# Optimization experiments

Hardware: AMD Instinct MI355X
Metric: run time of the kernel (lower is better)

Reference implementation:

```python
import jax, jax.numpy as jnp
import numpy as np

OUT_H = OUT_W = 7
SCALE = 0.25
SR = 2  # sampling_ratio


def setup_inputs() -> dict:
    key = jax.random.key(0)
    k1, k2, k3, k4, k5, k6 = jax.random.split(key, 6)
    B, C, H, W = 2, 256, 200, 304
    N = 1000
    inputs = jax.random.normal(k1, (B, C, H, W), dtype=jnp.float32)
    # rois: (batch_idx, cx, cy, w, h, angle_deg) in IMAGE coords (scale back by 1/SCALE)
    bidx = jax.random.randint(k2, (N,), 0, B).astype(jnp.float32)
    cx = jax.random.uniform(k3, (N,), minval=0.0, maxval=W / SCALE)
    cy = jax.random.uniform(k4, (N,), minval=0.0, maxval=H / SCALE)
    wh = jax.random.uniform(k5, (N, 2), minval=16.0, maxval=256.0)
    ang = jax.random.uniform(k6, (N,), minval=-90.0, maxval=90.0)
    rois = jnp.concatenate([bidx[:, None], cx[:, None], cy[:, None], wh, ang[:, None]], axis=1)
    return {"inputs": inputs, "rois": rois}


def _roi_align_rotated(feats, rois):
    B, C, H, W = feats.shape
    N = rois.shape[0]
    offset = 0.5  # aligned=True continuous-coordinate convention
    bidx = rois[:, 0].astype(jnp.int32)
    cw = rois[:, 1] * SCALE - offset
    ch = rois[:, 2] * SCALE - offset
    rw = rois[:, 3] * SCALE
    rh = rois[:, 4] * SCALE
    theta = rois[:, 5] * (jnp.pi / 180.0)
    cos_t, sin_t = jnp.cos(theta), jnp.sin(theta)

    bin_h = rh / OUT_H
    bin_w = rw / OUT_W
    # fused (bin, subsample) coordinate: t[j] = ph + (iy+0.5)/SR for j = ph*SR+iy
    t_y = (jnp.arange(OUT_H * SR, dtype=feats.dtype) + 0.5) / SR  # [GH]
    t_x = (jnp.arange(OUT_W * SR, dtype=feats.dtype) + 0.5) / SR  # [GW]
    yy = -rh[:, None] / 2.0 + t_y[None, :] * bin_h[:, None]  # [N,GH] roi-local
    xx = -rw[:, None] / 2.0 + t_x[None, :] * bin_w[:, None]  # [N,GW]

    # rotate into feature-map coords
    y = yy[:, :, None] * cos_t[:, None, None] - xx[:, None, :] * sin_t[:, None, None] + ch[:, None, None]
    x = yy[:, :, None] * sin_t[:, None, None] + xx[:, None, :] * cos_t[:, None, None] + cw[:, None, None]

    empty = (y < -1.0) | (y > H) | (x < -1.0) | (x > W)
    y = jnp.clip(y, 0.0, None)
    x = jnp.clip(x, 0.0, None)
    y_low = jnp.clip(jnp.floor(y).astype(jnp.int32), 0, H - 1)
    x_low = jnp.clip(jnp.floor(x).astype(jnp.int32), 0, W - 1)
    y_high = jnp.minimum(y_low + 1, H - 1)
    x_high = jnp.minimum(x_low + 1, W - 1)
    ly = jnp.clip(y - y_low.astype(y.dtype), 0.0, 1.0)
    lx = jnp.clip(x - x_low.astype(x.dtype), 0.0, 1.0)
    hy, hx = 1.0 - ly, 1.0 - lx

    b = bidx[:, None, None]  # [N,1,1] broadcasts with [N,GH,GW] index arrays
    v1 = feats[b, :, y_low, x_low]    # [N,GH,GW,C]
    v2 = feats[b, :, y_low, x_high]
    v3 = feats[b, :, y_high, x_low]
    v4 = feats[b, :, y_high, x_high]

    w1 = (hy * hx)[..., None]
    w2 = (hy * lx)[..., None]
    w3 = (ly * hx)[..., None]
    w4 = (ly * lx)[..., None]
    val = w1 * v1 + w2 * v2 + w3 * v3 + w4 * v4  # [N,GH,GW,C]
    val = jnp.where(empty[..., None], 0.0, val)

    # average the SRxSR samples within each output bin
    val = val.reshape(rois.shape[0], OUT_H, SR, OUT_W, SR, C).mean(axis=(2, 4))
    return jnp.transpose(val, (0, 3, 1, 2))  # [N,C,OUT_H,OUT_W]


def reference(inputs, rois):
    return _roi_align_rotated(inputs, rois)
```

## Files before the change

kernel.cpp:

```cpp
#include <hip/hip_runtime.h>
#include <math.h>

constexpr int Bn = 2, Cn = 256, Hn = 200, Wn = 304, Nroi = 1000;
constexpr int OH = 7, OW = 7, SRn = 2;
constexpr int NS = OH * SRn;
constexpr int NP = NS * NS;
constexpr int NBIN = OH * OW;
constexpr int HWn = Hn * Wn;
constexpr float SCALE = 0.25f;

__device__ __forceinline__ void compute_desc(const float* __restrict__ r, int p,
                                             int& idx, int& dx, int& dyW,
                                             float4& w) {
  float cw = r[1] * SCALE - 0.5f;
  float ch = r[2] * SCALE - 0.5f;
  float rw = r[3] * SCALE;
  float rh = r[4] * SCALE;
  float theta = r[5] * 0.017453292519943295f;
  float cs = cosf(theta), sn = sinf(theta);
  float bin_h = rh * (1.0f / OH);
  float bin_w = rw * (1.0f / OW);
  int ki = p / NS;
  int kj = p - ki * NS;
  float ty = ((float)ki + 0.5f) * (1.0f / SRn);
  float tx = ((float)kj + 0.5f) * (1.0f / SRn);
  float yy = -0.5f * rh + ty * bin_h;
  float xx = -0.5f * rw + tx * bin_w;
  float y = yy * cs - xx * sn + ch;
  float x = yy * sn + xx * cs + cw;
  bool empty = (y < -1.0f) || (y > (float)Hn) || (x < -1.0f) || (x > (float)Wn);
  y = fmaxf(y, 0.0f);
  x = fmaxf(x, 0.0f);
  int yl = min(max((int)floorf(y), 0), Hn - 1);
  int xl = min(max((int)floorf(x), 0), Wn - 1);
  int yh = min(yl + 1, Hn - 1);
  int xh = min(xl + 1, Wn - 1);
  float ly = fminf(fmaxf(y - (float)yl, 0.0f), 1.0f);
  float lx = fminf(fmaxf(x - (float)xl, 0.0f), 1.0f);
  float hy = 1.0f - ly, hx = 1.0f - lx;
  if (empty) {
    w.x = w.y = w.z = w.w = 0.0f;
  } else {
    w.x = hy * hx;
    w.y = hy * lx;
    w.z = ly * hx;
    w.w = ly * lx;
  }
  idx = yl * Wn + xl;
  dx = xh - xl;
  dyW = (yh - yl) * Wn;
}

__device__ __forceinline__ unsigned bf16rne(float f) {
  unsigned u = __float_as_uint(f);
  return (u + 0x7fffu + ((u >> 16) & 1u)) >> 16;
}
__device__ __forceinline__ unsigned bf16pack(float lo, float hi) {
  return bf16rne(lo) | (bf16rne(hi) << 16);
}

__global__ __launch_bounds__(512) void sort_rois(const float* __restrict__ rois,
                                                 int* __restrict__ perm) {
  __shared__ unsigned a[1024];
  int t = threadIdx.x;
  for (int i = t; i < 1024; i += 512) {
    unsigned packed;
    if (i < Nroi) {
      const float* r = rois + (size_t)i * 6;
      int b = (int)r[0];
      int tx = min(max((int)(r[1] * SCALE * (1.0f / 16.0f)), 0), 31);
      int ty = min(max((int)(r[2] * SCALE * (1.0f / 16.0f)), 0), 31);
      unsigned m = 0;
#pragma unroll
      for (int bit = 0; bit < 5; ++bit) {
        m |= (((tx >> bit) & 1u) << (2 * bit)) | (((ty >> bit) & 1u) << (2 * bit + 1));
      }
      unsigned key = ((unsigned)b << 10) | m;
      packed = (key << 10) | (unsigned)i;
    } else {
      packed = 0xFFFFFC00u | (unsigned)i;
    }
    a[i] = packed;
  }
  for (int k = 2; k <= 1024; k <<= 1) {
    for (int j = k >> 1; j > 0; j >>= 1) {
      __syncthreads();
      int i = ((t & ~(j - 1)) << 1) | (t & (j - 1));
      bool up = ((i & k) == 0);
      unsigned x = a[i], y = a[i + j];
      if ((x > y) == up) {
        a[i] = y;
        a[i + j] = x;
      }
    }
  }
  __syncthreads();
  for (int i = t; i < Nroi; i += 512) perm[i] = (int)(a[i] & 1023u);
}

constexpr int TPX = 64, TCH = 64, LP = TPX + 1;
__global__ __launch_bounds__(256) void transpose_bf16(const float* __restrict__ feats,
                                                      unsigned short* __restrict__ ft) {
  __shared__ float tile[TCH * LP];
  int p0 = blockIdx.x * TPX;
  int c0 = blockIdx.y * TCH;
  int b = blockIdx.z;
  int t = threadIdx.x;
  int px4 = t & 15, ch = t >> 4;
#pragma unroll
  for (int i = 0; i < 4; ++i) {
    int c = ch + 16 * i;
    const float4 v = *(const float4*)(feats + ((size_t)b * Cn + c0 + c) * HWn + p0 + px4 * 4);
    tile[c * LP + px4 * 4 + 0] = v.x;
    tile[c * LP + px4 * 4 + 1] = v.y;
    tile[c * LP + px4 * 4 + 2] = v.z;
    tile[c * LP + px4 * 4 + 3] = v.w;
  }
  __syncthreads();
  int o = t & 7;
  int px8 = t >> 3;
#pragma unroll
  for (int pass = 0; pass < 2; ++pass) {
    int p = px8 + 32 * pass;
    uint4 w4;
    w4.x = bf16pack(tile[(o * 8 + 0) * LP + p], tile[(o * 8 + 1) * LP + p]);
    w4.y = bf16pack(tile[(o * 8 + 2) * LP + p], tile[(o * 8 + 3) * LP + p]);
    w4.z = bf16pack(tile[(o * 8 + 4) * LP + p], tile[(o * 8 + 5) * LP + p]);
    w4.w = bf16pack(tile[(o * 8 + 6) * LP + p], tile[(o * 8 + 7) * LP + p]);
    *(uint4*)((char*)ft + (((size_t)b * HWn + p0 + p) * Cn + c0 + o * 8) * 2) = w4;
  }
}

constexpr int BPX = 32;
constexpr int SEG = 125;
__global__ __launch_bounds__(512, 2) void roi_gather9(const unsigned short* __restrict__ ft,
                                                      const float* __restrict__ rois,
                                                      const int* __restrict__ perm,
                                                      float* __restrict__ out) {
  __shared__ int4 s_m[NP];
  __shared__ float4 s_w[NP];
  __shared__ __align__(16) float s_out[Cn * NBIN];
  int x = blockIdx.x & 7;
  int jb = blockIdx.x >> 3;
  int t = threadIdx.x;
  int lane = t & 63;
  int wv = t >> 6;
  int k = lane & 31;
  int q = lane >> 5;

  for (int step = 0; step < 4; ++step) {
    int idxr = step * BPX + jb;
    if (idxr >= SEG) break;
    int n = perm[x * SEG + idxr];
    const float* r = rois + (size_t)n * 6;
    if (t < NP) {
      int idx, dx, dy;
      float4 w;
      compute_desc(r, t, idx, dx, dy, w);
      s_m[t] = make_int4(idx * (Cn * 2), dx * (Cn * 2), dy * (Cn * 2), 0);
      s_w[t] = w;
    }
    __syncthreads();
    int b = (int)r[0];
    const char* fb = (const char*)ft + (size_t)b * HWn * Cn * 2 + (size_t)k * 16;

    for (int bin = wv; bin < NBIN; bin += 8) {
      int bi = bin / OW;
      int bj = bin - bi * OW;
      int p00 = (bi * 2) * NS + bj * 2;
      float acc0 = 0.f, acc1 = 0.f, acc2 = 0.f, acc3 = 0.f;
      float acc4 = 0.f, acc5 = 0.f, acc6 = 0.f, acc7 = 0.f;
#pragma unroll
      for (int s = 0; s < 4; ++s) {
        int p = p00 + (s >> 1) * NS + (s & 1);
        int4 m = s_m[p];
        float4 w = s_w[p];
        const char* A = fb + m.x + q * m.y;
        uint4 vlo = *(const uint4*)(A);
        uint4 vhi = *(const uint4*)(A + m.z);
        float wlo = q ? w.y : w.x;
        float whi = q ? w.w : w.z;
#define ACC(vv, ww)                                                        \
        acc0 += (ww) * __uint_as_float((vv).x << 16);                      \
        acc1 += (ww) * __uint_as_float((vv).x & 0xffff0000u);              \
        acc2 += (ww) * __uint_as_float((vv).y << 16);                      \
        acc3 += (ww) * __uint_as_float((vv).y & 0xffff0000u);              \
        acc4 += (ww) * __uint_as_float((vv).z << 16);                      \
        acc5 += (ww) * __uint_as_float((vv).z & 0xffff0000u);              \
        acc6 += (ww) * __uint_as_float((vv).w << 16);                      \
        acc7 += (ww) * __uint_as_float((vv).w & 0xffff0000u);
        ACC(vlo, wlo)
        ACC(vhi, whi)
#undef ACC
      }
      acc0 += __shfl_xor(acc0, 32);
      acc1 += __shfl_xor(acc1, 32);
      acc2 += __shfl_xor(acc2, 32);
      acc3 += __shfl_xor(acc3, 32);
      acc4 += __shfl_xor(acc4, 32);
      acc5 += __shfl_xor(acc5, 32);
      acc6 += __shfl_xor(acc6, 32);
      acc7 += __shfl_xor(acc7, 32);
      if (q == 0) {
        s_out[(k * 8 + 0) * NBIN + bin] = acc0 * 0.25f;
        s_out[(k * 8 + 1) * NBIN + bin] = acc1 * 0.25f;
        s_out[(k * 8 + 2) * NBIN + bin] = acc2 * 0.25f;
        s_out[(k * 8 + 3) * NBIN + bin] = acc3 * 0.25f;
        s_out[(k * 8 + 4) * NBIN + bin] = acc4 * 0.25f;
        s_out[(k * 8 + 5) * NBIN + bin] = acc5 * 0.25f;
        s_out[(k * 8 + 6) * NBIN + bin] = acc6 * 0.25f;
        s_out[(k * 8 + 7) * NBIN + bin] = acc7 * 0.25f;
      }
    }
    __syncthreads();
    float* ob = out + (size_t)n * Cn * NBIN;
    for (int i = t; i < Cn * NBIN; i += 512) ob[i] = s_out[i];
    __syncthreads();
  }
}

__global__ __launch_bounds__(256) void roi_direct(const float* __restrict__ feats,
                                                  const float* __restrict__ rois,
                                                  float* __restrict__ out) {
  __shared__ int s_idx[NP];
  __shared__ int s_dx[NP];
  __shared__ int s_dy[NP];
  __shared__ float4 s_w[NP];
  int n = blockIdx.x;
  const float* r = rois + (size_t)n * 6;
  int t = threadIdx.x;
  if (t < NP) {
    int idx, dx, dy;
    float4 w;
    compute_desc(r, t, idx, dx, dy, w);
    s_idx[t] = idx;
    s_dx[t] = dx;
    s_dy[t] = dy;
    s_w[t] = w;
  }
  __syncthreads();
  int b = (int)r[0];
  const float* f = feats + ((size_t)b * Cn + t) * HWn;
  float* o = out + ((size_t)n * Cn + t) * NBIN;
  for (int bi = 0; bi < OH; ++bi) {
    for (int bj = 0; bj < OW; ++bj) {
      float acc = 0.0f;
#pragma unroll
      for (int s = 0; s < 4; ++s) {
        int p = (bi * 2 + (s >> 1)) * NS + bj * 2 + (s & 1);
        int idx = s_idx[p];
        int dx = s_dx[p];
        int dy = s_dy[p];
        float4 w = s_w[p];
        acc += w.x * f[idx] + w.y * f[idx + dx] + w.z * f[idx + dy] + w.w * f[idx + dy + dx];
      }
      o[bi * OW + bj] = acc * 0.25f;
    }
  }
}

extern "C" void kernel_launch(void* const* d_in, const int* in_sizes, int n_in,
                              void* d_out, int out_size, void* d_ws, size_t ws_size,
                              hipStream_t stream) {
  const float* feats = (const float*)d_in[0];
  const float* rois = (const float*)d_in[1];
  float* out = (float*)d_out;

  size_t ftBytes = (size_t)Bn * HWn * Cn * sizeof(unsigned short);
  size_t need = ftBytes + 4096;
  if (ws_size >= need) {
    unsigned short* ft = (unsigned short*)d_ws;
    int* perm = (int*)((char*)d_ws + ftBytes);
    sort_rois<<<1, 512, 0, stream>>>(rois, perm);
    transpose_bf16<<<dim3(HWn / TPX, Cn / TCH, Bn), 256, 0, stream>>>(feats, ft);
    roi_gather9<<<dim3(8 * BPX), 512, 0, stream>>>(ft, rois, perm, out);
  } else {
    roi_direct<<<Nroi, 256, 0, stream>>>(feats, rois, out);
  }
}
```

Before: 244.8 us.

## Split ROI gather across channel groups with smaller blocks and more grid parallelism

Replaces the 256-block, 512-thread gather kernel, which looped over ROIs with all 256 channels per block, with a 256-thread kernel launched as 63 ROI groups times 8 channel groups of 32 channels, each block handling 16 sorted ROIs. Each lane now loads one 16-byte corner and the four corners are reduced with two xor shuffles, so one wave covers 4 bins at a time. The goal is more blocks and higher occupancy through smaller shared memory and more parallel gathers. The cost is that sampling descriptors are recomputed once per channel group, there are more syncthreads per ROI, and lanes for the padded 49th-plus bins do wasted work.

Result: slower. 297.5 us (+21.5%).

```diff
diff --git a/kernel.cpp b/kernel.cpp
--- a/kernel.cpp
+++ b/kernel.cpp
@@ -131,27 +131,28 @@
   }
 }
 
-constexpr int BPX = 32;
-constexpr int SEG = 125;
-__global__ __launch_bounds__(512, 2) void roi_gather9(const unsigned short* __restrict__ ft,
-                                                      const float* __restrict__ rois,
-                                                      const int* __restrict__ perm,
-                                                      float* __restrict__ out) {
+constexpr int RPB = 16;
+constexpr int NG = (Nroi + RPB - 1) / RPB;
+__global__ __launch_bounds__(256, 4) void roi_gather10(const unsigned short* __restrict__ ft,
+                                                       const float* __restrict__ rois,
+                                                       const int* __restrict__ perm,
+                                                       float* __restrict__ out) {
   __shared__ int4 s_m[NP];
   __shared__ float4 s_w[NP];
-  __shared__ __align__(16) float s_out[Cn * NBIN];
-  int x = blockIdx.x & 7;
-  int jb = blockIdx.x >> 3;
+  __shared__ float s_out[32 * NBIN];
+  int cgrp = blockIdx.x & 7;
+  int gidx = blockIdx.x >> 3;
+  int c0 = cgrp * 32;
   int t = threadIdx.x;
   int lane = t & 63;
   int wv = t >> 6;
-  int k = lane & 31;
-  int q = lane >> 5;
-
-  for (int step = 0; step < 4; ++step) {
-    int idxr = step * BPX + jb;
-    if (idxr >= SEG) break;
-    int n = perm[x * SEG + idxr];
+  int cc = lane & 3;
+  int rq = (lane >> 2) & 3;
+  int b2 = lane >> 4;
+
+  int roiEnd = min(Nroi - gidx * RPB, RPB);
+  for (int j = 0; j < roiEnd; ++j) {
+    int n = perm[gidx * RPB + j];
     const float* r = rois + (size_t)n * 6;
     if (t < NP) {
       int idx, dx, dy;
@@ -162,59 +163,61 @@
     }
     __syncthreads();
     int b = (int)r[0];
-    const char* fb = (const char*)ft + (size_t)b * HWn * Cn * 2 + (size_t)k * 16;
-
-    for (int bin = wv; bin < NBIN; bin += 8) {
-      int bi = bin / OW;
-      int bj = bin - bi * OW;
+    const char* base = (const char*)ft + ((size_t)b * HWn * Cn + c0 + cc * 8) * 2;
+
+    for (int bin0 = wv * 4; bin0 < NBIN; bin0 += 16) {
+      int bin = bin0 + b2;
+      bool valid = bin < NBIN;
+      int binc = valid ? bin : (NBIN - 1);
+      int bi = binc / OW;
+      int bj = binc - bi * OW;
       int p00 = (bi * 2) * NS + bj * 2;
-      float acc0 = 0.f, acc1 = 0.f, acc2 = 0.f, acc3 = 0.f;
-      float acc4 = 0.f, acc5 = 0.f, acc6 = 0.f, acc7 = 0.f;
+      float a0 = 0.f, a1 = 0.f, a2 = 0.f, a3 = 0.f;
+      float a4 = 0.f, a5 = 0.f, a6 = 0.f, a7 = 0.f;
 #pragma unroll
       for (int s = 0; s < 4; ++s) {
         int p = p00 + (s >> 1) * NS + (s & 1);
         int4 m = s_m[p];
         float4 w = s_w[p];
-        const char* A = fb + m.x + q * m.y;
-        uint4 vlo = *(const uint4*)(A);
-        uint4 vhi = *(const uint4*)(A + m.z);
-        float wlo = q ? w.y : w.x;
-        float whi = q ? w.w : w.z;
-#define ACC(vv, ww)                                                        \
-        acc0 += (ww) * __uint_as_float((vv).x << 16);                      \
-        acc1 += (ww) * __uint_as_float((vv).x & 0xffff0000u);              \
-        acc2 += (ww) * __uint_as_float((vv).y << 16);                      \
-        acc3 += (ww) * __uint_as_float((vv).y & 0xffff0000u);              \
-        acc4 += (ww) * __uint_as_float((vv).z << 16);                      \
-        acc5 += (ww) * __uint_as_float((vv).z & 0xffff0000u);              \
-        acc6 += (ww) * __uint_as_float((vv).w << 16);                      \
-        acc7 += (ww) * __uint_as_float((vv).w & 0xffff0000u);
-        ACC(vlo, wlo)
-        ACC(vhi, whi)
-#undef ACC
-      }
-      acc0 += __shfl_xor(acc0, 32);
-      acc1 += __shfl_xor(acc1, 32);
-      acc2 += __shfl_xor(acc2, 32);
-      acc3 += __shfl_xor(acc3, 32);
-      acc4 += __shfl_xor(acc4, 32);
-      acc5 += __shfl_xor(acc5, 32);
-      acc6 += __shfl_xor(acc6, 32);
-      acc7 += __shfl_xor(acc7, 32);
-      if (q == 0) {
-        s_out[(k * 8 + 0) * NBIN + bin] = acc0 * 0.25f;
-        s_out[(k * 8 + 1) * NBIN + bin] = acc1 * 0.25f;
-        s_out[(k * 8 + 2) * NBIN + bin] = acc2 * 0.25f;
-        s_out[(k * 8 + 3) * NBIN + bin] = acc3 * 0.25f;
-        s_out[(k * 8 + 4) * NBIN + bin] = acc4 * 0.25f;
-        s_out[(k * 8 + 5) * NBIN + bin] = acc5 * 0.25f;
-        s_out[(k * 8 + 6) * NBIN + bin] = acc6 * 0.25f;
-        s_out[(k * 8 + 7) * NBIN + bin] = acc7 * 0.25f;
+        const char* A = base + m.x + ((rq & 1) ? m.y : 0) + ((rq & 2) ? m.z : 0);
+        uint4 v = *(const uint4*)A;
+        float wgt = (rq & 1) ? ((rq & 2) ? w.w : w.y) : ((rq & 2) ? w.z : w.x);
+        if (!valid) wgt = 0.f;
+        a0 += wgt * __uint_as_float(v.x << 16);
+        a1 += wgt * __uint_as_float(v.x & 0xffff0000u);
+        a2 += wgt * __uint_as_float(v.y << 16);
+        a3 += wgt * __uint_as_float(v.y & 0xffff0000u);
+        a4 += wgt * __uint_as_float(v.z << 16);
+        a5 += wgt * __uint_as_float(v.z & 0xffff0000u);
+        a6 += wgt * __uint_as_float(v.w << 16);
+        a7 += wgt * __uint_as_float(v.w & 0xffff0000u);
+      }
+#define RED(msk)                     \
+      a0 += __shfl_xor(a0, msk);     \
+      a1 += __shfl_xor(a1, msk);     \
+      a2 += __shfl_xor(a2, msk);     \
+      a3 += __shfl_xor(a3, msk);     \
+      a4 += __shfl_xor(a4, msk);     \
+      a5 += __shfl_xor(a5, msk);     \
+      a6 += __shfl_xor(a6, msk);     \
+      a7 += __shfl_xor(a7, msk);
+      RED(4)
+      RED(8)
+#undef RED
+      if (rq == 0 && valid) {
+        s_out[(cc * 8 + 0) * NBIN + bin] = a0 * 0.25f;
+        s_out[(cc * 8 + 1) * NBIN + bin] = a1 * 0.25f;
+        s_out[(cc * 8 + 2) * NBIN + bin] = a2 * 0.25f;
+        s_out[(cc * 8 + 3) * NBIN + bin] = a3 * 0.25f;
+        s_out[(cc * 8 + 4) * NBIN + bin] = a4 * 0.25f;
+        s_out[(cc * 8 + 5) * NBIN + bin] = a5 * 0.25f;
+        s_out[(cc * 8 + 6) * NBIN + bin] = a6 * 0.25f;
+        s_out[(cc * 8 + 7) * NBIN + bin] = a7 * 0.25f;
       }
     }
     __syncthreads();
-    float* ob = out + (size_t)n * Cn * NBIN;
-    for (int i = t; i < Cn * NBIN; i += 512) ob[i] = s_out[i];
+    float* og = out + ((size_t)n * Cn + c0) * NBIN;
+    for (int i = t; i < 32 * NBIN; i += 256) og[i] = s_out[i];
     __syncthreads();
   }
 }
@@ -273,7 +276,7 @@
     int* perm = (int*)((char*)d_ws + ftBytes);
     sort_rois<<<1, 512, 0, stream>>>(rois, perm);
     transpose_bf16<<<dim3(HWn / TPX, Cn / TCH, Bn), 256, 0, stream>>>(feats, ft);
-    roi_gather9<<<dim3(8 * BPX), 512, 0, stream>>>(ft, rois, perm, out);
+    roi_gather10<<<dim3(NG * 8), 256, 0, stream>>>(ft, rois, perm, out);
   } else {
     roi_direct<<<Nroi, 256, 0, stream>>>(feats, rois, out);
   }
```
